# Kernel tuning notes

Hardware: AMD Instinct MI355X
Metric: run time of the kernel (lower is better)

## Reference

```python
import jax, jax.numpy as jnp
import numpy as np

# Kernel codes matching style 'L;O2;P2;Y2,1,1;R0.5;W1,1'
KERNEL_CODES = ['L', 'O', 'P', 'Y', 'R', 'W']
SM_TEMP = 1.0


def _norm_sq(q, k):
    # q: [n,l,h,e], k: [n,s,h,e] -> [n,h,l,s]
    q2 = jnp.einsum('nlhe,nlhe->nhl', q, q)[..., None]        # [n,h,l,1]
    k2 = jnp.einsum('nshe,nshe->nhs', k, k)[:, :, None, :]     # [n,h,1,s]
    qk = jnp.einsum('nlhe,nshe->nhls', q, k)
    return q2 + k2 - 2.0 * qk


def _kernel(code, q, k):
    if code == 'L':
        return jnp.einsum('nlhe,nshe->nhls', q, k)
    if code == 'O':  # -log(1 + ns^(p/2)), p=2
        return -jnp.log1p(_norm_sq(q, k))
    if code == 'P':  # -(ns)^(p/2), p=2
        return -_norm_sq(q, k)
    if code == 'Y':  # (alpha*<q,k> + c)^p, p=2, alpha=1, c=1
        d = jnp.einsum('nlhe,nshe->nhls', q, k)
        return (d + 1.0) ** 2
    if code == 'R':  # exp(-gamma*ns), gamma=0.5
        return jnp.exp(-0.5 * _norm_sq(q, k))
    if code == 'W':  # cos(ns/a)*exp(-ns/b), a=b=1
        ns = _norm_sq(q, k)
        return jnp.cos(ns) * jnp.exp(-ns)
    raise ValueError(code)


def setup_inputs() -> dict:
    key = jax.random.key(0)
    k1, k2, k3, k4 = jax.random.split(key, 4)
    N, L, S, H, E, K = 2, 1024, 1024, 8, 64, 6
    return {
        'query': jax.random.normal(k1, (N, L, H, E), dtype=jnp.float32),
        'key': jax.random.normal(k2, (N, S, H, E), dtype=jnp.float32),
        'attn_mask_add': jnp.zeros((N, L, S), dtype=jnp.float32),
        'key_lengths_add': jnp.zeros((N, S), dtype=jnp.float32),
        'M': jax.random.uniform(k3, (H, E, K), dtype=jnp.float32),
        'C': jax.random.uniform(k4, (K, H, E, E), dtype=jnp.float32),
    }


def reference(query, key, attn_mask_add, key_lengths_add, M, C):
    # mixture weights pi: [n,l,h,k]
    pi = jax.nn.softmax(jnp.einsum('nlhe,hek->nlhk', query, M), axis=-1)
    out = None
    for c, code in enumerate(KERNEL_CODES):
        # htilde = tanh(query @ C[c]): [n,l,h,e]
        htilde = jnp.tanh(jnp.einsum('nlhe,hef->nlhf', query, C[c]))
        qk = _kernel(code, htilde, key)                    # [n,h,l,s]
        qk = qk + attn_mask_add[:, None] + key_lengths_add[:, None, None, :]
        sm = jax.nn.softmax(SM_TEMP * qk, axis=-1)
        w = jnp.transpose(pi[..., c], (0, 2, 1))[..., None]  # [n,h,l,1]
        term = sm * w
        out = term if out is None else out + term
    return out
```

## Files before the change

kernel.cpp:

```cpp
#include <hip/hip_runtime.h>
#include <hip/hip_bf16.h>
#include <math.h>

#define N_  2
#define H_  8
#define G_  16
#define L_  1024
#define S_  1024
#define E_  64
#define NC_ 6

typedef __attribute__((ext_vector_type(4))) float floatx4;
typedef __attribute__((ext_vector_type(8))) short short8;

#define MFMA16 __builtin_amdgcn_mfma_f32_16x16x32_bf16

#define AHAT_OFF   0
#define AHAT_BYTES (NC_*G_*L_*128*2)
#define KHAT_OFF   (AHAT_OFF + AHAT_BYTES)
#define KHAT_BYTES (G_*S_*128*2)
#define PI_OFF     (KHAT_OFF + KHAT_BYTES)
#define PI_BYTES   (NC_*G_*L_*4)
#define HSQ_OFF    (PI_OFF + PI_BYTES)
#define HSQ_BYTES  (NC_*G_*L_*4)
#define KSQ_OFF    (HSQ_OFF + HSQ_BYTES)
#define KSQ_BYTES  (G_*S_*4)

__global__ __launch_bounds__(256) void k_prep_a(
    const float* __restrict__ q, const float* __restrict__ M,
    const float* __restrict__ C, __hip_bfloat16* __restrict__ Ahat,
    float* __restrict__ pi_t, float* __restrict__ hsq) {
  extern __shared__ char smraw[];
  float* qs    = (float*)smraw;
  float* Cs    = qs + 32*65;
  float* hsq_s = Cs + 3*4104;
  float* pm    = hsq_s + 6*32;

  int b  = blockIdx.x;
  int n  = b >> 8; int h = (b >> 5) & 7; int lc = b & 31;
  int l0 = lc * 32; int g = n*8 + h;
  int t  = threadIdx.x;

  if (t < 192) hsq_s[t] = 0.0f;
  {
    int u = t;
    #pragma unroll
    for (int rep = 0; rep < 2; rep++, u += 256) {
      int row = u >> 4, seg = u & 15;
      float4 v = *(const float4*)(q + (((size_t)(n*L_ + l0 + row))*H_ + h)*E_ + seg*4);
      float* dst = qs + row*65 + seg*4;
      dst[0]=v.x; dst[1]=v.y; dst[2]=v.z; dst[3]=v.w;
    }
  }
  for (int gc = 0; gc < 2; gc++) {
    __syncthreads();
    for (int u = t; u < 3072; u += 256) {
      int cc = u >> 10; int rem = u & 1023; int e = rem >> 4; int seg = rem & 15;
      float4 v = *(const float4*)(C + (((size_t)((gc*3+cc)*8 + h))*64 + e)*64 + seg*4);
      float* dst = Cs + cc*4104 + e*64 + seg*4;
      dst[0]=v.x; dst[1]=v.y; dst[2]=v.z; dst[3]=v.w;
    }
    __syncthreads();
    if (t < 192) {
      int cc = t >> 6; int tt = t & 63; int lg = tt >> 3; int fg = tt & 7;
      int c = gc*3 + cc;
      float acc[4][8];
      #pragma unroll
      for (int i = 0; i < 4; i++)
        #pragma unroll
        for (int j = 0; j < 8; j++) acc[i][j] = 0.0f;
      for (int e = 0; e < 64; e++) {
        float c8[8];
        #pragma unroll
        for (int j = 0; j < 8; j++) c8[j] = Cs[cc*4104 + e*64 + fg*8 + j];
        #pragma unroll
        for (int i = 0; i < 4; i++) {
          float qv = qs[(lg*4+i)*65 + e];
          #pragma unroll
          for (int j = 0; j < 8; j++) acc[i][j] = fmaf(qv, c8[j], acc[i][j]);
        }
      }
      #pragma unroll
      for (int i = 0; i < 4; i++) {
        int l = l0 + lg*4 + i;
        size_t rowb = (((size_t)(c*G_ + g))*L_ + l) * 128;
        float ss = 0.0f;
        short8 hi8, lo8;
        #pragma unroll
        for (int j = 0; j < 8; j++) {
          float hv = tanhf(acc[i][j]);
          ss += hv*hv;
          __hip_bfloat16 hi = __float2bfloat16(hv);
          __hip_bfloat16 lo = __float2bfloat16(hv - __bfloat162float(hi));
          short hs, ls;
          __builtin_memcpy(&hs, &hi, 2);
          __builtin_memcpy(&ls, &lo, 2);
          hi8[j] = hs; lo8[j] = ls;
        }
        *(short8*)((char*)Ahat + (rowb + fg*8)*2)      = hi8;
        *(short8*)((char*)Ahat + (rowb + 64 + fg*8)*2) = lo8;
        atomicAdd(&hsq_s[c*32 + lg*4 + i], ss);
      }
    }
  }
  if (t < 192) {
    int k = t >> 5; int l = t & 31;
    float p = 0.0f;
    for (int e = 0; e < 64; e++) p += qs[l*65 + e] * M[(h*64 + e)*6 + k];
    pm[l*8 + k] = p;
  }
  __syncthreads();
  if (t < 192) {
    int k = t >> 5; int l = t & 31;
    float mx = pm[l*8+0];
    #pragma unroll
    for (int kk = 1; kk < 6; kk++) mx = fmaxf(mx, pm[l*8+kk]);
    float den = 0.0f;
    #pragma unroll
    for (int kk = 0; kk < 6; kk++) den += __expf(pm[l*8+kk] - mx);
    float pv = __expf(pm[l*8+k] - mx) / den;
    size_t idx = ((size_t)(k*G_ + g))*L_ + l0 + l;
    pi_t[idx] = pv;
    hsq[idx]  = hsq_s[k*32 + l];
  }
}

__global__ __launch_bounds__(256) void k_prep_k(
    const float* __restrict__ key, __hip_bfloat16* __restrict__ Khat,
    float* __restrict__ ksq) {
  int t = threadIdx.x; int wv = t >> 6; int lane = t & 63;
  int r = blockIdx.x*4 + wv;
  int g = r >> 10; int s = r & 1023; int n = g >> 3; int h = g & 7;
  float v = key[(((size_t)(n*S_ + s))*H_ + h)*E_ + lane];
  __hip_bfloat16 hi = __float2bfloat16(v);
  __hip_bfloat16 lo = __float2bfloat16(v - __bfloat162float(hi));
  size_t base = ((size_t)g*S_ + s)*128;
  Khat[base + lane]      = hi;
  Khat[base + 64 + lane] = lo;
  float sq = v*v;
  #pragma unroll
  for (int off = 32; off; off >>= 1) sq += __shfl_xor(sq, off);
  if (lane == 0) ksq[(size_t)g*S_ + s] = sq;
}

#define LDS_A6    0
#define LDS_K     0
#define LDS_KSQ   17408
#define LDS_KLEN  17664
#define LDS_ZRED  24576
#define LDS_MRED  26112
#define LDS_CST   27648
#define LDS_HSQ   28416
#define LDS_PI    28800
#define LDS_TOTAL 29184

__global__ __launch_bounds__(256, 2) void k_main(
    const __hip_bfloat16* __restrict__ Ahat, const __hip_bfloat16* __restrict__ Khat,
    const float* __restrict__ hsq, const float* __restrict__ ksq,
    const float* __restrict__ mask, const float* __restrict__ klen,
    const float* __restrict__ pi_t, float* __restrict__ out) {
  extern __shared__ char smraw[];
  char*   A6     = smraw + LDS_A6;
  char*   K_lds  = smraw + LDS_K;
  float*  ksq_t  = (float*)(smraw + LDS_KSQ);
  float*  klen_t = (float*)(smraw + LDS_KLEN);
  float*  zred   = (float*)(smraw + LDS_ZRED);
  float*  mred   = (float*)(smraw + LDS_MRED);
  float2* cst    = (float2*)(smraw + LDS_CST);
  float*  hsq_s  = (float*)(smraw + LDS_HSQ);
  float*  pi_s   = (float*)(smraw + LDS_PI);

  const int l0 = blockIdx.x * 16; const int g = blockIdx.y; const int n = g >> 3;
  const int t = threadIdx.x; const int w = t >> 6; const int lane = t & 63;
  const int quad = lane >> 4; const int lc = lane & 15;

  #pragma unroll
  for (int rep = 0; rep < 6; rep++) {
    int u = t + rep*256; int cc = u >> 8; int rem = u & 255;
    int row = rem >> 4; int seg = rem & 15;
    *(int4*)(A6 + cc*4096 + row*256 + seg*16) =
      *(const int4*)((const char*)Ahat + (((size_t)(cc*G_+g))*L_ + l0 + row)*256 + seg*16);
  }
  if (t < 96) {
    size_t idx = ((size_t)((t >> 4)*G_ + g))*L_ + l0 + (t & 15);
    hsq_s[t] = hsq[idx];
    pi_s[t]  = pi_t[idx];
  }
  __syncthreads();

  short8 a6f[6][4];
  #pragma unroll
  for (int cc = 0; cc < 6; cc++)
    #pragma unroll
    for (int kt = 0; kt < 4; kt++)
      a6f[cc][kt] = *(const short8*)(A6 + cc*4096 + lc*256 + kt*64 + quad*16);

  float h1p[4], nh2[4], h4h[4], nh5[4];
  #pragma unroll
  for (int i = 0; i < 4; i++) {
    int r = quad*4 + i;
    h1p[i] = 1.0f + hsq_s[1*16 + r];
    nh2[i] = -hsq_s[2*16 + r];
    h4h[i] = -0.5f * hsq_s[4*16 + r];
    nh5[i] = -hsq_s[5*16 + r];
  }

  float Zc[4][4];
  float m2[4], z2[4], m3[4], z3[4];
  #pragma unroll
  for (int i = 0; i < 4; i++) {
    #pragma unroll
    for (int c = 0; c < 4; c++) Zc[c][i] = 0.0f;
    m2[i] = -INFINITY; z2[i] = 0.0f;
    m3[i] = -INFINITY; z3[i] = 0.0f;
  }

  #pragma unroll 1
  for (int st = 0; st < 16; st++) {
    int s0 = st*64;
    __syncthreads();
    #pragma unroll
    for (int rep = 0; rep < 4; rep++) {
      int u = t + rep*256; int row = u >> 4, seg = u & 15;
      *(int4*)(K_lds + row*272 + seg*16) =
        *(const int4*)((const char*)Khat + (((size_t)g)*S_ + s0 + row)*256 + seg*16);
    }
    if (t < 64) { ksq_t[t] = ksq[(size_t)g*S_ + s0 + t]; klen_t[t] = klen[(size_t)n*S_ + s0 + t]; }
    int scol = s0 + w*16 + lc;
    float mk[4];
    #pragma unroll
    for (int i = 0; i < 4; i++)
      mk[i] = mask[((size_t)(n*L_ + l0 + quad*4 + i))*S_ + scol];
    __syncthreads();
    short8 bfr[4];
    #pragma unroll
    for (int kt = 0; kt < 4; kt++)
      bfr[kt] = *(const short8*)(K_lds + (w*16 + lc)*272 + kt*64 + quad*16);
    float kq  = ksq_t[w*16 + lc];
    float klv = klen_t[w*16 + lc];
    float mv[4], Ev[4];
    #pragma unroll
    for (int i = 0; i < 4; i++) { mv[i] = mk[i] + klv; Ev[i] = __expf(mv[i]); }
    #pragma unroll
    for (int c = 0; c < 6; c++) {
      floatx4 a = {0.f, 0.f, 0.f, 0.f};
      a = MFMA16(a6f[c][0], bfr[0], a, 0,0,0);
      a = MFMA16(a6f[c][1], bfr[1], a, 0,0,0);
      a = MFMA16(a6f[c][0], bfr[2], a, 0,0,0);
      a = MFMA16(a6f[c][1], bfr[3], a, 0,0,0);
      a = MFMA16(a6f[c][2], bfr[0], a, 0,0,0);
      a = MFMA16(a6f[c][3], bfr[1], a, 0,0,0);
      #pragma unroll
      for (int i = 0; i < 4; i++) {
        float d = a[i];
        if (c == 0) {
          Zc[0][i] = fmaf(Ev[i], __expf(d), Zc[0][i]);
        } else if (c == 1) {
          float onep = fmaf(-2.f, d, h1p[i] + kq);
          Zc[1][i] = fmaf(Ev[i], __builtin_amdgcn_rcpf(onep), Zc[1][i]);
        } else if (c == 2) {
          float x  = fmaf(2.f, d, nh2[i] - kq) + mv[i];
          float mn = fmaxf(m2[i], x);
          float e  = __expf(fminf(m2[i], x) - mn);
          z2[i] = (x > m2[i]) ? fmaf(z2[i], e, 1.0f) : (z2[i] + e);
          m2[i] = mn;
        } else if (c == 3) {
          float tt = d + 1.f;
          float x  = fmaf(tt, tt, mv[i]);
          float mn = fmaxf(m3[i], x);
          float e  = __expf(fminf(m3[i], x) - mn);
          z3[i] = (x > m3[i]) ? fmaf(z3[i], e, 1.0f) : (z3[i] + e);
          m3[i] = mn;
        } else if (c == 4) {
          float a4 = d + fmaf(-0.5f, kq, h4h[i]);
          Zc[2][i] = fmaf(Ev[i], __expf(__expf(a4)), Zc[2][i]);
        } else {
          float a5 = fmaf(2.f, d, nh5[i] - kq);
          Zc[3][i] = fmaf(Ev[i], __expf(__cosf(a5) * __expf(a5)), Zc[3][i]);
        }
      }
    }
  }

  #pragma unroll
  for (int off = 1; off < 16; off <<= 1) {
    #pragma unroll
    for (int c = 0; c < 4; c++)
      #pragma unroll
      for (int i = 0; i < 4; i++) Zc[c][i] += __shfl_xor(Zc[c][i], off);
    #pragma unroll
    for (int i = 0; i < 4; i++) {
      float mo = __shfl_xor(m2[i], off);
      float zo = __shfl_xor(z2[i], off);
      float mn = fmaxf(m2[i], mo);
      float e  = __expf(fminf(m2[i], mo) - mn);
      z2[i] = (mo > m2[i]) ? fmaf(z2[i], e, zo) : fmaf(zo, e, z2[i]);
      m2[i] = mn;
      mo = __shfl_xor(m3[i], off);
      zo = __shfl_xor(z3[i], off);
      mn = fmaxf(m3[i], mo);
      e  = __expf(fminf(m3[i], mo) - mn);
      z3[i] = (mo > m3[i]) ? fmaf(z3[i], e, zo) : fmaf(zo, e, z3[i]);
      m3[i] = mn;
    }
  }
  if (lc == 0) {
    static const int cmap[4] = {0, 1, 4, 5};
    #pragma unroll
    for (int c = 0; c < 4; c++)
      #pragma unroll
      for (int i = 0; i < 4; i++) {
        zred[w*96 + cmap[c]*16 + quad*4 + i] = Zc[c][i];
        mred[w*96 + cmap[c]*16 + quad*4 + i] = 0.f;
      }
    #pragma unroll
    for (int i = 0; i < 4; i++) {
      zred[w*96 + 2*16 + quad*4 + i] = z2[i];
      mred[w*96 + 2*16 + quad*4 + i] = m2[i];
      zred[w*96 + 3*16 + quad*4 + i] = z3[i];
      mred[w*96 + 3*16 + quad*4 + i] = m3[i];
    }
  }
  __syncthreads();
  if (t < 96) {
    int c = t >> 4;
    float z = zred[t], m = mred[t];
    if (c == 2 || c == 3) {
      #pragma unroll
      for (int w2 = 1; w2 < 4; w2++) {
        float mo = mred[w2*96 + t], zo = zred[w2*96 + t];
        float mn = fmaxf(m, mo);
        float e  = __expf(fminf(m, mo) - mn);
        z = (mo > m) ? fmaf(z, e, zo) : fmaf(zo, e, z);
        m = mn;
      }
    } else {
      #pragma unroll
      for (int w2 = 1; w2 < 4; w2++) z += zred[w2*96 + t];
    }
    cst[t] = make_float2(pi_s[t] / z, m);
  }
  __syncthreads();

  float ac[6][4], m2f[4], m3f[4];
  #pragma unroll
  for (int c = 0; c < 6; c++)
    #pragma unroll
    for (int i = 0; i < 4; i++) {
      float2 v = cst[c*16 + quad*4 + i];
      ac[c][i] = v.x;
      if (c == 2) m2f[i] = v.y;
      if (c == 3) m3f[i] = v.y;
    }

  #pragma unroll 1
  for (int st = 0; st < 16; st++) {
    int s0 = st*64;
    __syncthreads();
    #pragma unroll
    for (int rep = 0; rep < 4; rep++) {
      int u = t + rep*256; int row = u >> 4, seg = u & 15;
      *(int4*)(K_lds + row*272 + seg*16) =
        *(const int4*)((const char*)Khat + (((size_t)g)*S_ + s0 + row)*256 + seg*16);
    }
    if (t < 64) { ksq_t[t] = ksq[(size_t)g*S_ + s0 + t]; klen_t[t] = klen[(size_t)n*S_ + s0 + t]; }
    int scol = s0 + w*16 + lc;
    float mk[4];
    #pragma unroll
    for (int i = 0; i < 4; i++)
      mk[i] = mask[((size_t)(n*L_ + l0 + quad*4 + i))*S_ + scol];
    __syncthreads();
    short8 bfr[4];
    #pragma unroll
    for (int kt = 0; kt < 4; kt++)
      bfr[kt] = *(const short8*)(K_lds + (w*16 + lc)*272 + kt*64 + quad*16);
    float kq  = ksq_t[w*16 + lc];
    float klv = klen_t[w*16 + lc];
    float mv[4], Ev[4];
    #pragma unroll
    for (int i = 0; i < 4; i++) { mv[i] = mk[i] + klv; Ev[i] = __expf(mv[i]); }
    float Sacc[4] = {0.f, 0.f, 0.f, 0.f};
    float G[4]    = {0.f, 0.f, 0.f, 0.f};
    #pragma unroll
    for (int c = 0; c < 6; c++) {
      floatx4 a = {0.f, 0.f, 0.f, 0.f};
      a = MFMA16(a6f[c][0], bfr[0], a, 0,0,0);
      a = MFMA16(a6f[c][1], bfr[1], a, 0,0,0);
      a = MFMA16(a6f[c][0], bfr[2], a, 0,0,0);
      a = MFMA16(a6f[c][1], bfr[3], a, 0,0,0);
      a = MFMA16(a6f[c][2], bfr[0], a, 0,0,0);
      a = MFMA16(a6f[c][3], bfr[1], a, 0,0,0);
      #pragma unroll
      for (int i = 0; i < 4; i++) {
        float d = a[i];
        if (c == 0) {
          Sacc[i] = fmaf(ac[0][i], __expf(d), Sacc[i]);
        } else if (c == 1) {
          float onep = fmaf(-2.f, d, h1p[i] + kq);
          Sacc[i] = fmaf(ac[1][i], __builtin_amdgcn_rcpf(onep), Sacc[i]);
        } else if (c == 2) {
          float x = fmaf(2.f, d, nh2[i] - kq) + mv[i];
          G[i] = fmaf(ac[2][i], __expf(x - m2f[i]), G[i]);
        } else if (c == 3) {
          float tt = d + 1.f;
          float x  = fmaf(tt, tt, mv[i]);
          G[i] = fmaf(ac[3][i], __expf(x - m3f[i]), G[i]);
        } else if (c == 4) {
          float a4 = d + fmaf(-0.5f, kq, h4h[i]);
          Sacc[i] = fmaf(ac[4][i], __expf(__expf(a4)), Sacc[i]);
        } else {
          float a5 = fmaf(2.f, d, nh5[i] - kq);
          Sacc[i] = fmaf(ac[5][i], __expf(__cosf(a5) * __expf(a5)), Sacc[i]);
        }
      }
    }
    #pragma unroll
    for (int i = 0; i < 4; i++)
      out[(((size_t)g)*L_ + l0 + quad*4 + i)*S_ + scol] = fmaf(Ev[i], Sacc[i], G[i]);
  }
}

extern "C" void kernel_launch(void* const* d_in, const int* in_sizes, int n_in,
                              void* d_out, int out_size, void* d_ws, size_t ws_size,
                              hipStream_t stream) {
  (void)in_sizes; (void)n_in; (void)out_size; (void)ws_size;
  const float* q    = (const float*)d_in[0];
  const float* key  = (const float*)d_in[1];
  const float* mask = (const float*)d_in[2];
  const float* klen = (const float*)d_in[3];
  const float* M    = (const float*)d_in[4];
  const float* C    = (const float*)d_in[5];
  char* ws = (char*)d_ws;
  __hip_bfloat16* Ahat = (__hip_bfloat16*)(ws + AHAT_OFF);
  __hip_bfloat16* Khat = (__hip_bfloat16*)(ws + KHAT_OFF);
  float* pi_t    = (float*)(ws + PI_OFF);
  float* hsq     = (float*)(ws + HSQ_OFF);
  float* ksq     = (float*)(ws + KSQ_OFF);
  float* out = (float*)d_out;

  k_prep_a<<<512, 256, 59360, stream>>>(q, M, C, Ahat, pi_t, hsq);
  k_prep_k<<<4096, 256, 0, stream>>>(key, Khat, ksq);
  k_main<<<dim3(64, 16), 256, LDS_TOTAL, stream>>>(Ahat, Khat, hsq, ksq, mask, klen,
                                                   pi_t, out);
}
```

Measured before the change: 241.9 us.

## Double-buffer K tiles via registers, merge prep kernels, use fixed shift for P softmax

The key preprocessing kernel is folded into the query prep kernel, saving one launch. In the main kernel, K tiles plus ksq, klen and mask values are prefetched into registers one step ahead and written to alternating LDS buffers, which drops one barrier per step and overlaps global loads with MFMA work. The online max tracking for the P kernel (c==2) is replaced by a constant shift of 64, which removes per-element max/rescale work. That shift assumes the fixed-offset exponent stays in float range, which holds for tanh-bounded queries with E=64 but could overflow or underflow for general masks or inputs.

```diff
diff --git a/kernel.cpp b/kernel.cpp
--- a/kernel.cpp
+++ b/kernel.cpp
@@ -26,10 +26,11 @@
 #define KSQ_OFF    (HSQ_OFF + HSQ_BYTES)
 #define KSQ_BYTES  (G_*S_*4)
 
-__global__ __launch_bounds__(256) void k_prep_a(
-    const float* __restrict__ q, const float* __restrict__ M,
-    const float* __restrict__ C, __hip_bfloat16* __restrict__ Ahat,
-    float* __restrict__ pi_t, float* __restrict__ hsq) {
+__global__ __launch_bounds__(256) void k_prep(
+    const float* __restrict__ q, const float* __restrict__ key,
+    const float* __restrict__ M, const float* __restrict__ C,
+    __hip_bfloat16* __restrict__ Ahat, __hip_bfloat16* __restrict__ Khat,
+    float* __restrict__ ksq, float* __restrict__ pi_t, float* __restrict__ hsq) {
   extern __shared__ char smraw[];
   float* qs    = (float*)smraw;
   float* Cs    = qs + 32*65;
@@ -40,6 +41,25 @@
   int n  = b >> 8; int h = (b >> 5) & 7; int lc = b & 31;
   int l0 = lc * 32; int g = n*8 + h;
   int t  = threadIdx.x;
+
+  {
+    int wv = t >> 6; int lane = t & 63;
+    #pragma unroll
+    for (int j = 0; j < 8; j++) {
+      int r = b*32 + wv*8 + j;
+      int kg = r >> 10; int s = r & 1023; int kn = kg >> 3; int kh = kg & 7;
+      float v = key[(((size_t)(kn*S_ + s))*H_ + kh)*E_ + lane];
+      __hip_bfloat16 hi = __float2bfloat16(v);
+      __hip_bfloat16 lo = __float2bfloat16(v - __bfloat162float(hi));
+      size_t base = ((size_t)kg*S_ + s)*128;
+      Khat[base + lane]      = hi;
+      Khat[base + 64 + lane] = lo;
+      float sq = v*v;
+      #pragma unroll
+      for (int off = 32; off; off >>= 1) sq += __shfl_xor(sq, off);
+      if (lane == 0) ksq[(size_t)kg*S_ + s] = sq;
+    }
+  }
 
   if (t < 192) hsq_s[t] = 0.0f;
   {
@@ -125,34 +145,14 @@
   }
 }
 
-__global__ __launch_bounds__(256) void k_prep_k(
-    const float* __restrict__ key, __hip_bfloat16* __restrict__ Khat,
-    float* __restrict__ ksq) {
-  int t = threadIdx.x; int wv = t >> 6; int lane = t & 63;
-  int r = blockIdx.x*4 + wv;
-  int g = r >> 10; int s = r & 1023; int n = g >> 3; int h = g & 7;
-  float v = key[(((size_t)(n*S_ + s))*H_ + h)*E_ + lane];
-  __hip_bfloat16 hi = __float2bfloat16(v);
-  __hip_bfloat16 lo = __float2bfloat16(v - __bfloat162float(hi));
-  size_t base = ((size_t)g*S_ + s)*128;
-  Khat[base + lane]      = hi;
-  Khat[base + 64 + lane] = lo;
-  float sq = v*v;
-  #pragma unroll
-  for (int off = 32; off; off >>= 1) sq += __shfl_xor(sq, off);
-  if (lane == 0) ksq[(size_t)g*S_ + s] = sq;
-}
-
-#define LDS_A6    0
-#define LDS_K     0
-#define LDS_KSQ   17408
-#define LDS_KLEN  17664
-#define LDS_ZRED  24576
-#define LDS_MRED  26112
-#define LDS_CST   27648
-#define LDS_HSQ   28416
-#define LDS_PI    28800
-#define LDS_TOTAL 29184
+#define LDS_BUF0  0
+#define LDS_BUF1  17408
+#define LDS_ZRED  34816
+#define LDS_MRED  36352
+#define LDS_CST   37888
+#define LDS_HSQ   38656
+#define LDS_PI    39040
+#define LDS_TOTAL 39424
 
 __global__ __launch_bounds__(256, 2) void k_main(
     const __hip_bfloat16* __restrict__ Ahat, const __hip_bfloat16* __restrict__ Khat,
@@ -160,10 +160,7 @@
     const float* __restrict__ mask, const float* __restrict__ klen,
     const float* __restrict__ pi_t, float* __restrict__ out) {
   extern __shared__ char smraw[];
-  char*   A6     = smraw + LDS_A6;
-  char*   K_lds  = smraw + LDS_K;
-  float*  ksq_t  = (float*)(smraw + LDS_KSQ);
-  float*  klen_t = (float*)(smraw + LDS_KLEN);
+  char*   A6     = smraw;
   float*  zred   = (float*)(smraw + LDS_ZRED);
   float*  mred   = (float*)(smraw + LDS_MRED);
   float2* cst    = (float2*)(smraw + LDS_CST);
@@ -173,6 +170,7 @@
   const int l0 = blockIdx.x * 16; const int g = blockIdx.y; const int n = g >> 3;
   const int t = threadIdx.x; const int w = t >> 6; const int lane = t & 63;
   const int quad = lane >> 4; const int lc = lane & 15;
+  const char* Kg = (const char*)Khat + ((size_t)g)*S_*256;
 
   #pragma unroll
   for (int rep = 0; rep < 6; rep++) {
@@ -200,47 +198,76 @@
   for (int i = 0; i < 4; i++) {
     int r = quad*4 + i;
     h1p[i] = 1.0f + hsq_s[1*16 + r];
-    nh2[i] = -hsq_s[2*16 + r];
+    nh2[i] = 64.0f - hsq_s[2*16 + r];
     h4h[i] = -0.5f * hsq_s[4*16 + r];
     nh5[i] = -hsq_s[5*16 + r];
   }
-
-  float Zc[4][4];
-  float m2[4], z2[4], m3[4], z3[4];
+  __syncthreads();
+
+  float Zc[4][4], zp[4];
+  float m3[4], z3[4];
   #pragma unroll
   for (int i = 0; i < 4; i++) {
     #pragma unroll
     for (int c = 0; c < 4; c++) Zc[c][i] = 0.0f;
-    m2[i] = -INFINITY; z2[i] = 0.0f;
-    m3[i] = -INFINITY; z3[i] = 0.0f;
-  }
+    zp[i] = 0.0f; m3[i] = -INFINITY; z3[i] = 0.0f;
+  }
+
+  const int scol_base = w*16 + lc;
+  int4 kreg[4];
+  float mkN[4], kqN, klvN;
+
+  #pragma unroll
+  for (int rep = 0; rep < 4; rep++) {
+    int u = t + rep*256; int row = u >> 4, seg = u & 15;
+    kreg[rep] = *(const int4*)(Kg + (size_t)row*256 + seg*16);
+  }
+  kqN  = ksq[(size_t)g*S_ + scol_base];
+  klvN = klen[(size_t)n*S_ + scol_base];
+  #pragma unroll
+  for (int i = 0; i < 4; i++)
+    mkN[i] = mask[((size_t)(n*L_ + l0 + quad*4 + i))*S_ + scol_base];
 
   #pragma unroll 1
   for (int st = 0; st < 16; st++) {
-    int s0 = st*64;
-    __syncthreads();
+    char* buf = smraw + ((st & 1) ? LDS_BUF1 : LDS_BUF0);
     #pragma unroll
     for (int rep = 0; rep < 4; rep++) {
       int u = t + rep*256; int row = u >> 4, seg = u & 15;
-      *(int4*)(K_lds + row*272 + seg*16) =
-        *(const int4*)((const char*)Khat + (((size_t)g)*S_ + s0 + row)*256 + seg*16);
-    }
-    if (t < 64) { ksq_t[t] = ksq[(size_t)g*S_ + s0 + t]; klen_t[t] = klen[(size_t)n*S_ + s0 + t]; }
-    int scol = s0 + w*16 + lc;
-    float mk[4];
-    #pragma unroll
-    for (int i = 0; i < 4; i++)
-      mk[i] = mask[((size_t)(n*L_ + l0 + quad*4 + i))*S_ + scol];
+      *(int4*)(buf + row*272 + seg*16) = kreg[rep];
+    }
+    float kq = kqN, klv = klvN;
+    float mv[4];
+    #pragma unroll
+    for (int i = 0; i < 4; i++) mv[i] = mkN[i] + klv;
     __syncthreads();
+    if (st < 15) {
+      int s1 = (st+1)*64;
+      #pragma unroll
+      for (int rep = 0; rep < 4; rep++) {
+        int u = t + rep*256; int row = u >> 4, seg = u & 15;
+        kreg[rep] = *(const int4*)(Kg + (size_t)(s1 + row)*256 + seg*16);
+      }
+      int sc1 = s1 + scol_base;
+      kqN  = ksq[(size_t)g*S_ + sc1];
+      klvN = klen[(size_t)n*S_ + sc1];
+      #pragma unroll
+      for (int i = 0; i < 4; i++)
+        mkN[i] = mask[((size_t)(n*L_ + l0 + quad*4 + i))*S_ + sc1];
+    }
     short8 bfr[4];
     #pragma unroll
     for (int kt = 0; kt < 4; kt++)
-      bfr[kt] = *(const short8*)(K_lds + (w*16 + lc)*272 + kt*64 + quad*16);
-    float kq  = ksq_t[w*16 + lc];
-    float klv = klen_t[w*16 + lc];
-    float mv[4], Ev[4];
-    #pragma unroll
-    for (int i = 0; i < 4; i++) { mv[i] = mk[i] + klv; Ev[i] = __expf(mv[i]); }
+      bfr[kt] = *(const short8*)(buf + (w*16 + lc)*272 + kt*64 + quad*16);
+    float Ev[4], oc[4], pc[4], rc[4], wc[4];
+    #pragma unroll
+    for (int i = 0; i < 4; i++) {
+      Ev[i] = __expf(mv[i]);
+      oc[i] = h1p[i] + kq;
+      pc[i] = nh2[i] - kq + mv[i];
+      rc[i] = fmaf(-0.5f, kq, h4h[i]);
+      wc[i] = nh5[i] - kq;
+    }
     #pragma unroll
     for (int c = 0; c < 6; c++) {
       floatx4 a = {0.f, 0.f, 0.f, 0.f};
@@ -256,14 +283,9 @@
         if (c == 0) {
           Zc[0][i] = fmaf(Ev[i], __expf(d), Zc[0][i]);
         } else if (c == 1) {
-          float onep = fmaf(-2.f, d, h1p[i] + kq);
-          Zc[1][i] = fmaf(Ev[i], __builtin_amdgcn_rcpf(onep), Zc[1][i]);
+          Zc[1][i] = fmaf(Ev[i], __builtin_amdgcn_rcpf(fmaf(-2.f, d, oc[i])), Zc[1][i]);
         } else if (c == 2) {
-          float x  = fmaf(2.f, d, nh2[i] - kq) + mv[i];
-          float mn = fmaxf(m2[i], x);
-          float e  = __expf(fminf(m2[i], x) - mn);
-          z2[i] = (x > m2[i]) ? fmaf(z2[i], e, 1.0f) : (z2[i] + e);
-          m2[i] = mn;
+          zp[i] += __expf(fmaf(2.f, d, pc[i]));
         } else if (c == 3) {
           float tt = d + 1.f;
           float x  = fmaf(tt, tt, mv[i]);
@@ -272,10 +294,9 @@
           z3[i] = (x > m3[i]) ? fmaf(z3[i], e, 1.0f) : (z3[i] + e);
           m3[i] = mn;
         } else if (c == 4) {
-          float a4 = d + fmaf(-0.5f, kq, h4h[i]);
-          Zc[2][i] = fmaf(Ev[i], __expf(__expf(a4)), Zc[2][i]);
+          Zc[2][i] = fmaf(Ev[i], __expf(__expf(d + rc[i])), Zc[2][i]);
         } else {
-          float a5 = fmaf(2.f, d, nh5[i] - kq);
+          float a5 = fmaf(2.f, d, wc[i]);
           Zc[3][i] = fmaf(Ev[i], __expf(__cosf(a5) * __expf(a5)), Zc[3][i]);
         }
       }
@@ -290,16 +311,11 @@
       for (int i = 0; i < 4; i++) Zc[c][i] += __shfl_xor(Zc[c][i], off);
     #pragma unroll
     for (int i = 0; i < 4; i++) {
-      float mo = __shfl_xor(m2[i], off);
-      float zo = __shfl_xor(z2[i], off);
-      float mn = fmaxf(m2[i], mo);
-      float e  = __expf(fminf(m2[i], mo) - mn);
-      z2[i] = (mo > m2[i]) ? fmaf(z2[i], e, zo) : fmaf(zo, e, z2[i]);
-      m2[i] = mn;
-      mo = __shfl_xor(m3[i], off);
-      zo = __shfl_xor(z3[i], off);
-      mn = fmaxf(m3[i], mo);
-      e  = __expf(fminf(m3[i], mo) - mn);
+      zp[i] += __shfl_xor(zp[i], off);
+      float mo = __shfl_xor(m3[i], off);
+      float zo = __shfl_xor(z3[i], off);
+      float mn = fmaxf(m3[i], mo);
+      float e  = __expf(fminf(m3[i], mo) - mn);
       z3[i] = (mo > m3[i]) ? fmaf(z3[i], e, zo) : fmaf(zo, e, z3[i]);
       m3[i] = mn;
     }
@@ -315,17 +331,27 @@
       }
     #pragma unroll
     for (int i = 0; i < 4; i++) {
-      zred[w*96 + 2*16 + quad*4 + i] = z2[i];
-      mred[w*96 + 2*16 + quad*4 + i] = m2[i];
+      zred[w*96 + 2*16 + quad*4 + i] = zp[i];
+      mred[w*96 + 2*16 + quad*4 + i] = 0.f;
       zred[w*96 + 3*16 + quad*4 + i] = z3[i];
       mred[w*96 + 3*16 + quad*4 + i] = m3[i];
     }
   }
+  #pragma unroll
+  for (int rep = 0; rep < 4; rep++) {
+    int u = t + rep*256; int row = u >> 4, seg = u & 15;
+    kreg[rep] = *(const int4*)(Kg + (size_t)row*256 + seg*16);
+  }
+  kqN  = ksq[(size_t)g*S_ + scol_base];
+  klvN = klen[(size_t)n*S_ + scol_base];
+  #pragma unroll
+  for (int i = 0; i < 4; i++)
+    mkN[i] = mask[((size_t)(n*L_ + l0 + quad*4 + i))*S_ + scol_base];
   __syncthreads();
   if (t < 96) {
     int c = t >> 4;
     float z = zred[t], m = mred[t];
-    if (c == 2 || c == 3) {
+    if (c == 3) {
       #pragma unroll
       for (int w2 = 1; w2 < 4; w2++) {
         float mo = mred[w2*96 + t], zo = zred[w2*96 + t];
@@ -342,43 +368,57 @@
   }
   __syncthreads();
 
-  float ac[6][4], m2f[4], m3f[4];
+  float ac[6][4], m3f[4];
   #pragma unroll
   for (int c = 0; c < 6; c++)
     #pragma unroll
     for (int i = 0; i < 4; i++) {
       float2 v = cst[c*16 + quad*4 + i];
       ac[c][i] = v.x;
-      if (c == 2) m2f[i] = v.y;
       if (c == 3) m3f[i] = v.y;
     }
 
   #pragma unroll 1
   for (int st = 0; st < 16; st++) {
-    int s0 = st*64;
-    __syncthreads();
+    char* buf = smraw + ((st & 1) ? LDS_BUF1 : LDS_BUF0);
     #pragma unroll
     for (int rep = 0; rep < 4; rep++) {
       int u = t + rep*256; int row = u >> 4, seg = u & 15;
-      *(int4*)(K_lds + row*272 + seg*16) =
-        *(const int4*)((const char*)Khat + (((size_t)g)*S_ + s0 + row)*256 + seg*16);
-    }
-    if (t < 64) { ksq_t[t] = ksq[(size_t)g*S_ + s0 + t]; klen_t[t] = klen[(size_t)n*S_ + s0 + t]; }
-    int scol = s0 + w*16 + lc;
-    float mk[4];
-    #pragma unroll
-    for (int i = 0; i < 4; i++)
-      mk[i] = mask[((size_t)(n*L_ + l0 + quad*4 + i))*S_ + scol];
+      *(int4*)(buf + row*272 + seg*16) = kreg[rep];
+    }
+    float kq = kqN, klv = klvN;
+    float mv[4];
+    #pragma unroll
+    for (int i = 0; i < 4; i++) mv[i] = mkN[i] + klv;
+    int scol = st*64 + scol_base;
     __syncthreads();
+    if (st < 15) {
+      int s1 = (st+1)*64;
+      #pragma unroll
+      for (int rep = 0; rep < 4; rep++) {
+        int u = t + rep*256; int row = u >> 4, seg = u & 15;
+        kreg[rep] = *(const int4*)(Kg + (size_t)(s1 + row)*256 + seg*16);
+      }
+      int sc1 = s1 + scol_base;
+      kqN  = ksq[(size_t)g*S_ + sc1];
+      klvN = klen[(size_t)n*S_ + sc1];
+      #pragma unroll
+      for (int i = 0; i < 4; i++)
+        mkN[i] = mask[((size_t)(n*L_ + l0 + quad*4 + i))*S_ + sc1];
+    }
     short8 bfr[4];
     #pragma unroll
     for (int kt = 0; kt < 4; kt++)
-      bfr[kt] = *(const short8*)(K_lds + (w*16 + lc)*272 + kt*64 + quad*16);
-    float kq  = ksq_t[w*16 + lc];
-    float klv = klen_t[w*16 + lc];
-    float mv[4], Ev[4];
-    #pragma unroll
-    for (int i = 0; i < 4; i++) { mv[i] = mk[i] + klv; Ev[i] = __expf(mv[i]); }
+      bfr[kt] = *(const short8*)(buf + (w*16 + lc)*272 + kt*64 + quad*16);
+    float Ev[4], oc[4], pc[4], rc[4], wc[4];
+    #pragma unroll
+    for (int i = 0; i < 4; i++) {
+      Ev[i] = __expf(mv[i]);
+      oc[i] = h1p[i] + kq;
+      pc[i] = nh2[i] - kq + mv[i];
+      rc[i] = fmaf(-0.5f, kq, h4h[i]);
+      wc[i] = nh5[i] - kq;
+    }
     float Sacc[4] = {0.f, 0.f, 0.f, 0.f};
     float G[4]    = {0.f, 0.f, 0.f, 0.f};
     #pragma unroll
@@ -396,20 +436,17 @@
         if (c == 0) {
           Sacc[i] = fmaf(ac[0][i], __expf(d), Sacc[i]);
         } else if (c == 1) {
-          float onep = fmaf(-2.f, d, h1p[i] + kq);
-          Sacc[i] = fmaf(ac[1][i], __builtin_amdgcn_rcpf(onep), Sacc[i]);
+          Sacc[i] = fmaf(ac[1][i], __builtin_amdgcn_rcpf(fmaf(-2.f, d, oc[i])), Sacc[i]);
         } else if (c == 2) {
-          float x = fmaf(2.f, d, nh2[i] - kq) + mv[i];
-          G[i] = fmaf(ac[2][i], __expf(x - m2f[i]), G[i]);
+          G[i] = fmaf(ac[2][i], __expf(fmaf(2.f, d, pc[i])), G[i]);
         } else if (c == 3) {
           float tt = d + 1.f;
           float x  = fmaf(tt, tt, mv[i]);
           G[i] = fmaf(ac[3][i], __expf(x - m3f[i]), G[i]);
         } else if (c == 4) {
-          float a4 = d + fmaf(-0.5f, kq, h4h[i]);
-          Sacc[i] = fmaf(ac[4][i], __expf(__expf(a4)), Sacc[i]);
+          Sacc[i] = fmaf(ac[4][i], __expf(__expf(d + rc[i])), Sacc[i]);
         } else {
-          float a5 = fmaf(2.f, d, nh5[i] - kq);
+          float a5 = fmaf(2.f, d, wc[i]);
           Sacc[i] = fmaf(ac[5][i], __expf(__cosf(a5) * __expf(a5)), Sacc[i]);
         }
       }
@@ -438,8 +475,7 @@
   float* ksq     = (float*)(ws + KSQ_OFF);
   float* out = (float*)d_out;
 
-  k_prep_a<<<512, 256, 59360, stream>>>(q, M, C, Ahat, pi_t, hsq);
-  k_prep_k<<<4096, 256, 0, stream>>>(key, Khat, ksq);
+  k_prep<<<512, 256, 59360, stream>>>(q, key, M, C, Ahat, Khat, ksq, pi_t, hsq);
   k_main<<<dim3(64, 16), 256, LDS_TOTAL, stream>>>(Ahat, Khat, hsq, ksq, mask, klen,
                                                    pi_t, out);
 }
```

After: 281.0 us. 16.2% more time.
